# Performance work log

Measured on AMD Instinct MI355X. Metric: run time of the kernel, lower is better.

## Reference

```python
import jax, jax.numpy as jnp
import numpy as np

MAX_LAG_FRACTION = 0.25
EPS = 1e-8
B, T = 1024, 2048


def setup_inputs() -> dict:
    key = jax.random.key(0)
    k1, k2, k3 = jax.random.split(key, 3)
    alpha_pred = jax.random.uniform(k1, (B,), dtype=jnp.float32)          # alpha in [0,1)
    D0_pred = jax.random.uniform(k2, (B,), dtype=jnp.float32)             # D0 in [0,1)
    trajectory = jax.random.normal(k3, (B, T, 2), dtype=jnp.float32)
    return {"alpha_pred": alpha_pred, "D0_pred": D0_pred, "trajectory": trajectory}


def _msd_all_lags(traj, max_lag):
    # traj: (B, T, C). Returns empirical MSD per sample per lag: (B, max_lag).
    Bn, Tn, _ = traj.shape
    t = jnp.arange(Tn)

    def step(carry, lag):
        idx = jnp.clip(t + lag, 0, Tn - 1)                    # (T,)
        disp = jnp.take(traj, idx, axis=1) - traj             # (B, T, C)
        sq = jnp.sum(disp * disp, axis=-1)                    # (B, T) squared displacement
        valid = (t + lag < Tn).astype(sq.dtype)               # (T,) mask for t in [0, T-lag)
        msd = jnp.sum(sq * valid[None, :], axis=-1) / jnp.maximum(jnp.sum(valid), 1.0)
        return carry, msd                                      # (B,)

    lags = jnp.arange(1, max_lag + 1)
    _, msd = jax.lax.scan(step, None, lags)                   # (max_lag, B)
    return msd.T                                               # (B, max_lag)


def reference(alpha_pred, D0_pred, trajectory):
    Bn, Tn, _ = trajectory.shape
    max_lag = max(1, int(Tn * MAX_LAG_FRACTION))
    msd_emp = _msd_all_lags(trajectory, max_lag)                               # (B, L)
    lags = jnp.arange(1, max_lag + 1, dtype=trajectory.dtype)                  # (L,)
    msd_theo = 4.0 * D0_pred[:, None] * jnp.power(lags[None, :], alpha_pred[:, None])  # (B, L)
    d = jnp.log(msd_theo + EPS) - jnp.log(msd_emp + EPS)
    # per-sample MSE over lags, then mean over batch (same as original loop)
    return jnp.mean(jnp.mean(d * d, axis=-1))
```

## Files before the change

kernel.cpp:

```cpp
#include <hip/hip_runtime.h>

#define B_SAMPLES 1024
#define T_LEN     2048
#define NLAG      512
#define ROWW      172

typedef _Float16 half8_t __attribute__((ext_vector_type(8)));
typedef float    floatx4 __attribute__((ext_vector_type(4)));

__device__ __forceinline__ int slotP(int k) { return k + (k >> 5); }

__global__ __launch_bounds__(256) void msd_mfma_kernel(
    const float* __restrict__ alpha, const float* __restrict__ d0p,
    const float* __restrict__ traj, float* __restrict__ partial) {
  const int b   = blockIdx.x;
  const int tid = threadIdx.x;
  const int w   = tid >> 6;
  const int l   = tid & 63;
  const int g   = l >> 4;
  const int p16 = l & 15;

  __shared__ __align__(16) unsigned int Zw[16 * ROWW];
  __shared__ float Pb[2116];
  __shared__ float Elds[33][16];
  __shared__ float wred[4];

  for (int k = tid; k < 16 * 44; k += 256)
    Zw[(k / 44) * ROWW + 128 + (k % 44)] = 0u;

  const float2* tr = reinterpret_cast<const float2*>(traj) + (size_t)b * T_LEN;
  #pragma unroll
  for (int s = 0; s < 8; ++s) {
    int t = (w << 9) + (s << 6) + l;
    float2 v2 = tr[t];
    _Float16 hx = (_Float16)v2.x;
    _Float16 hy = (_Float16)v2.y;
    unsigned int word = (unsigned int)__builtin_bit_cast(unsigned short, hx)
                      | ((unsigned int)__builtin_bit_cast(unsigned short, hy) << 16);
    Zw[(t & 15) * ROWW + (t >> 4)] = word;
  }
  __syncthreads();

  if (w == 0) {
    const unsigned int* zs = &Zw[2 * l];
    float csum = 0.f;
    #pragma unroll
    for (int i = 0; i < 32; ++i) {
      unsigned int word = zs[(i & 15) * ROWW + (i >> 4)];
      float fx = (float)__builtin_bit_cast(_Float16, (unsigned short)(word & 0xffffu));
      float fy = (float)__builtin_bit_cast(_Float16, (unsigned short)(word >> 16));
      csum = fmaf(fx, fx, fmaf(fy, fy, csum));
    }
    float run = csum;
    #pragma unroll
    for (int dlt = 1; dlt < 64; dlt <<= 1) {
      float tsh = __shfl_up(run, dlt, 64);
      if (l >= dlt) run += tsh;
    }
    float r2 = run - csum;
    if (l == 0) Pb[0] = 0.f;
    #pragma unroll
    for (int i = 0; i < 32; ++i) {
      unsigned int word = zs[(i & 15) * ROWW + (i >> 4)];
      float fx = (float)__builtin_bit_cast(_Float16, (unsigned short)(word & 0xffffu));
      float fy = (float)__builtin_bit_cast(_Float16, (unsigned short)(word >> 16));
      r2 = fmaf(fx, fx, fmaf(fy, fy, r2));
      Pb[slotP(32 * l + i + 1)] = r2;
    }
  }

  const unsigned int* zrow = &Zw[p16 * ROWW];
  const int vS = 8 * w;

  floatx4 D[9];
  #pragma unroll
  for (int r = 0; r < 9; ++r) D[r] = (floatx4){0.f, 0.f, 0.f, 0.f};

  #pragma unroll
  for (int q = 0; q < 8; ++q) {
    const unsigned int* wp = zrow + 16 * q + 4 * g + vS;
    uint4 w0 = *reinterpret_cast<const uint4*>(wp);
    uint4 w1 = *reinterpret_cast<const uint4*>(wp + 4);
    uint4 w2 = *reinterpret_cast<const uint4*>(wp + 8);
    unsigned int win[12] = {w0.x, w0.y, w0.z, w0.w,  w1.x, w1.y, w1.z, w1.w,
                            w2.x, w2.y, w2.z, w2.w};
    uint4 aw = *reinterpret_cast<const uint4*>(zrow + 16 * q + 4 * g);
    half8_t aq = __builtin_bit_cast(half8_t, aw);
    #pragma unroll
    for (int r = 0; r < 9; ++r) {
      uint4 bw;
      bw.x = win[r]; bw.y = win[r + 1]; bw.z = win[r + 2]; bw.w = win[r + 3];
      half8_t bf = __builtin_bit_cast(half8_t, bw);
      D[r] = __builtin_amdgcn_mfma_f32_16x16x32_f16(aq, bf, D[r], 0, 0, 0);
    }
  }

  float prevA = 0.f;
  const int rotb = 4 * g + p16;
  const int idx0 = (l & 48) << 2;

  #pragma unroll
  for (int r = 0; r < 9; ++r) {
    float accA = 0.f, accB = 0.f;
    #pragma unroll
    for (int rr = 0; rr < 4; ++rr) {
      float gv = D[r][rr];
      int src = idx0 | (((rotb + rr) & 15) << 2);
      float got = __builtin_bit_cast(float,
          __builtin_amdgcn_ds_bpermute(src, __builtin_bit_cast(int, gv)));
      bool wrap = (rotb + rr) >= 16;
      accA += wrap ? 0.f : got;
      accB += wrap ? got : 0.f;
    }
    if (r > 0) {
      float E = prevA + accB;
      E += __shfl_xor(E, 16, 64);
      E += __shfl_xor(E, 32, 64);
      if (l < 16) Elds[vS + r - 1][p16] = E;
    }
    prevA = accA;
  }
  if (w == 3) {
    float E = prevA;
    E += __shfl_xor(E, 16, 64);
    E += __shfl_xor(E, 32, 64);
    if (l == 0) Elds[32][0] = E;
  }
  __syncthreads();

  const float Ptot = Pb[slotP(2048)];
  const float aexp = alpha[b];
  const float c4d0 = 4.f * d0p[b];
  float loc = 0.f;
  #pragma unroll
  for (int c = 0; c < 2; ++c) {
    int lag = c * 256 + tid + 1;
    float E  = Elds[lag >> 4][lag & 15];
    float Pl = Pb[slotP(lag)];
    int mm   = 2048 - lag;
    float Pr = Pb[slotP(mm)];
    float S2  = Pr + (Ptot - Pl);
    float msd = fmaxf((S2 - 2.f * E) / (float)mm, 0.f);
    float theo = c4d0 * __builtin_exp2f(aexp * __builtin_log2f((float)lag));
    float dd = 0.69314718f * (__builtin_log2f(theo + 1e-8f) - __builtin_log2f(msd + 1e-8f));
    loc = fmaf(dd, dd, loc);
  }

  #pragma unroll
  for (int dlt = 1; dlt < 64; dlt <<= 1) loc += __shfl_xor(loc, dlt, 64);
  if (l == 0) wred[w] = loc;
  __syncthreads();
  if (tid == 0) partial[b] = (wred[0] + wred[1]) + (wred[2] + wred[3]);
}

__global__ __launch_bounds__(256) void reduce_kernel(
    const float* __restrict__ partial, float* __restrict__ out) {
  __shared__ float wsum[4];
  float acc = 0.f;
  for (int i = threadIdx.x; i < B_SAMPLES; i += 256) acc += partial[i];
  for (int off = 32; off > 0; off >>= 1) acc += __shfl_down(acc, off, 64);
  const int wid  = threadIdx.x >> 6;
  const int lane = threadIdx.x & 63;
  if (lane == 0) wsum[wid] = acc;
  __syncthreads();
  if (threadIdx.x == 0) {
    float t = wsum[0] + wsum[1] + wsum[2] + wsum[3];
    out[0] = t * (1.0f / ((float)B_SAMPLES * (float)NLAG));
  }
}

extern "C" void kernel_launch(void* const* d_in, const int* in_sizes, int n_in,
                              void* d_out, int out_size, void* d_ws, size_t ws_size,
                              hipStream_t stream) {
  const float* alpha = (const float*)d_in[0];
  const float* d0p   = (const float*)d_in[1];
  const float* traj  = (const float*)d_in[2];
  float* out     = (float*)d_out;
  float* partial = (float*)d_ws;

  msd_mfma_kernel<<<B_SAMPLES, 256, 0, stream>>>(alpha, d0p, traj, partial);
  reduce_kernel<<<1, 256, 0, stream>>>(partial, out);
}
```

Before: 15.90 us.

## Collapse per-sample block to one wavefront and drop block barriers

Each sample is now handled by a single 64-lane wavefront, not four waves. That one wave computes all 33 MFMA accumulator tiles, the prefix sums and all 512 lags, so every __syncthreads and the cross-wave reduction go away. Trajectory loads are widened to float4. The cost is far more accumulator registers per wave (33 floatx4) and less parallelism within a block, which may hurt latency hiding and occupancy. Dropping the barriers is safe only because every LDS producer and consumer now sits in the same wave.

```diff
diff --git a/kernel.cpp b/kernel.cpp
--- a/kernel.cpp
+++ b/kernel.cpp
@@ -10,38 +10,38 @@
 
 __device__ __forceinline__ int slotP(int k) { return k + (k >> 5); }
 
-__global__ __launch_bounds__(256) void msd_mfma_kernel(
+__global__ __launch_bounds__(64, 1) void msd_mfma_kernel(
     const float* __restrict__ alpha, const float* __restrict__ d0p,
     const float* __restrict__ traj, float* __restrict__ partial) {
   const int b   = blockIdx.x;
-  const int tid = threadIdx.x;
-  const int w   = tid >> 6;
-  const int l   = tid & 63;
+  const int l   = threadIdx.x;
   const int g   = l >> 4;
   const int p16 = l & 15;
 
   __shared__ __align__(16) unsigned int Zw[16 * ROWW];
   __shared__ float Pb[2116];
   __shared__ float Elds[33][16];
-  __shared__ float wred[4];
 
-  for (int k = tid; k < 16 * 44; k += 256)
+  for (int k = l; k < 16 * 44; k += 64)
     Zw[(k / 44) * ROWW + 128 + (k % 44)] = 0u;
 
-  const float2* tr = reinterpret_cast<const float2*>(traj) + (size_t)b * T_LEN;
+  const float4* tr4 = reinterpret_cast<const float4*>(traj) + (size_t)b * (T_LEN / 2);
   #pragma unroll
-  for (int s = 0; s < 8; ++s) {
-    int t = (w << 9) + (s << 6) + l;
-    float2 v2 = tr[t];
-    _Float16 hx = (_Float16)v2.x;
-    _Float16 hy = (_Float16)v2.y;
-    unsigned int word = (unsigned int)__builtin_bit_cast(unsigned short, hx)
-                      | ((unsigned int)__builtin_bit_cast(unsigned short, hy) << 16);
-    Zw[(t & 15) * ROWW + (t >> 4)] = word;
+  for (int s = 0; s < 16; ++s) {
+    int idx = (s << 6) + l;
+    float4 v4 = tr4[idx];
+    int t0 = idx << 1;
+    _Float16 hx0 = (_Float16)v4.x, hy0 = (_Float16)v4.y;
+    _Float16 hx1 = (_Float16)v4.z, hy1 = (_Float16)v4.w;
+    unsigned int wd0 = (unsigned int)__builtin_bit_cast(unsigned short, hx0)
+                     | ((unsigned int)__builtin_bit_cast(unsigned short, hy0) << 16);
+    unsigned int wd1 = (unsigned int)__builtin_bit_cast(unsigned short, hx1)
+                     | ((unsigned int)__builtin_bit_cast(unsigned short, hy1) << 16);
+    Zw[(t0 & 15) * ROWW + (t0 >> 4)] = wd0;
+    Zw[((t0 + 1) & 15) * ROWW + ((t0 + 1) >> 4)] = wd1;
   }
-  __syncthreads();
 
-  if (w == 0) {
+  {
     const unsigned int* zs = &Zw[2 * l];
     float csum = 0.f;
     #pragma unroll
@@ -70,24 +70,29 @@
   }
 
   const unsigned int* zrow = &Zw[p16 * ROWW];
-  const int vS = 8 * w;
+  floatx4 D[33];
+  #pragma unroll
+  for (int r = 0; r < 33; ++r) D[r] = (floatx4){0.f, 0.f, 0.f, 0.f};
 
-  floatx4 D[9];
-  #pragma unroll
-  for (int r = 0; r < 9; ++r) D[r] = (floatx4){0.f, 0.f, 0.f, 0.f};
-
-  #pragma unroll
   for (int q = 0; q < 8; ++q) {
-    const unsigned int* wp = zrow + 16 * q + 4 * g + vS;
+    const unsigned int* wp = zrow + 16 * q + 4 * g;
     uint4 w0 = *reinterpret_cast<const uint4*>(wp);
     uint4 w1 = *reinterpret_cast<const uint4*>(wp + 4);
     uint4 w2 = *reinterpret_cast<const uint4*>(wp + 8);
-    unsigned int win[12] = {w0.x, w0.y, w0.z, w0.w,  w1.x, w1.y, w1.z, w1.w,
-                            w2.x, w2.y, w2.z, w2.w};
-    uint4 aw = *reinterpret_cast<const uint4*>(zrow + 16 * q + 4 * g);
-    half8_t aq = __builtin_bit_cast(half8_t, aw);
+    uint4 w3 = *reinterpret_cast<const uint4*>(wp + 12);
+    uint4 w4 = *reinterpret_cast<const uint4*>(wp + 16);
+    uint4 w5 = *reinterpret_cast<const uint4*>(wp + 20);
+    uint4 w6 = *reinterpret_cast<const uint4*>(wp + 24);
+    uint4 w7 = *reinterpret_cast<const uint4*>(wp + 28);
+    uint4 w8 = *reinterpret_cast<const uint4*>(wp + 32);
+    unsigned int win[36] = {w0.x, w0.y, w0.z, w0.w,  w1.x, w1.y, w1.z, w1.w,
+                            w2.x, w2.y, w2.z, w2.w,  w3.x, w3.y, w3.z, w3.w,
+                            w4.x, w4.y, w4.z, w4.w,  w5.x, w5.y, w5.z, w5.w,
+                            w6.x, w6.y, w6.z, w6.w,  w7.x, w7.y, w7.z, w7.w,
+                            w8.x, w8.y, w8.z, w8.w};
+    half8_t aq = __builtin_bit_cast(half8_t, w0);
     #pragma unroll
-    for (int r = 0; r < 9; ++r) {
+    for (int r = 0; r < 33; ++r) {
       uint4 bw;
       bw.x = win[r]; bw.y = win[r + 1]; bw.z = win[r + 2]; bw.w = win[r + 3];
       half8_t bf = __builtin_bit_cast(half8_t, bw);
@@ -100,7 +105,7 @@
   const int idx0 = (l & 48) << 2;
 
   #pragma unroll
-  for (int r = 0; r < 9; ++r) {
+  for (int r = 0; r < 33; ++r) {
     float accA = 0.f, accB = 0.f;
     #pragma unroll
     for (int rr = 0; rr < 4; ++rr) {
@@ -116,25 +121,24 @@
       float E = prevA + accB;
       E += __shfl_xor(E, 16, 64);
       E += __shfl_xor(E, 32, 64);
-      if (l < 16) Elds[vS + r - 1][p16] = E;
+      if (l < 16) Elds[r - 1][p16] = E;
     }
     prevA = accA;
   }
-  if (w == 3) {
+  {
     float E = prevA;
     E += __shfl_xor(E, 16, 64);
     E += __shfl_xor(E, 32, 64);
     if (l == 0) Elds[32][0] = E;
   }
-  __syncthreads();
 
   const float Ptot = Pb[slotP(2048)];
   const float aexp = alpha[b];
   const float c4d0 = 4.f * d0p[b];
   float loc = 0.f;
   #pragma unroll
-  for (int c = 0; c < 2; ++c) {
-    int lag = c * 256 + tid + 1;
+  for (int c = 0; c < 8; ++c) {
+    int lag = (c << 6) + l + 1;
     float E  = Elds[lag >> 4][lag & 15];
     float Pl = Pb[slotP(lag)];
     int mm   = 2048 - lag;
@@ -148,9 +152,7 @@
 
   #pragma unroll
   for (int dlt = 1; dlt < 64; dlt <<= 1) loc += __shfl_xor(loc, dlt, 64);
-  if (l == 0) wred[w] = loc;
-  __syncthreads();
-  if (tid == 0) partial[b] = (wred[0] + wred[1]) + (wred[2] + wred[3]);
+  if (l == 0) partial[b] = loc;
 }
 
 __global__ __launch_bounds__(256) void reduce_kernel(
@@ -178,6 +180,6 @@
   float* out     = (float*)d_out;
   float* partial = (float*)d_ws;
 
-  msd_mfma_kernel<<<B_SAMPLES, 256, 0, stream>>>(alpha, d0p, traj, partial);
+  msd_mfma_kernel<<<B_SAMPLES, 64, 0, stream>>>(alpha, d0p, traj, partial);
   reduce_kernel<<<1, 256, 0, stream>>>(partial, out);
 }
```

Measured after the change: 19.44 us. 22.3% more time.
